# Kernel optimization log

Measured on AMD Instinct MI355X. Metric: run time of the kernel, lower is better.

The kernel has to match this reference:

```python
import jax, jax.numpy as jnp
import numpy as np

NUM_EMBEDDINGS = 1024
EMBEDDING_DIM = 64
COMMITMENT_WEIGHT = 0.25
BATCH = 262144


def setup_inputs() -> dict:
    key = jax.random.key(0)
    k1, k2 = jax.random.split(key)
    z = jax.random.normal(k1, (BATCH, EMBEDDING_DIM), dtype=jnp.float32)
    # torch init: uniform_(-1/K, 1/K)
    bound = 1.0 / NUM_EMBEDDINGS
    codebook = jax.random.uniform(k2, (NUM_EMBEDDINGS, EMBEDDING_DIM), dtype=jnp.float32,
                                  minval=-bound, maxval=bound)
    return {"z": z, "codebook": codebook}


def reference(z, codebook):
    # distances[b, k] = ||z_b||^2 - 2 z_b . c_k + ||c_k||^2   -> [B, K]
    z2 = jnp.sum(z * z, axis=1, keepdims=True)                 # [B, 1]
    c2 = jnp.sum(codebook * codebook, axis=1)                  # [K]
    cross = jnp.matmul(z, codebook.T)                          # [B, K]
    distances = z2 - 2.0 * cross + c2
    indices = jnp.argmin(distances, axis=1)                    # [B]
    # original uses one-hot @ codebook; direct gather is the same math
    z_q = codebook[indices]                                    # [B, D]
    commitment_loss = jnp.mean((jax.lax.stop_gradient(z_q) - z) ** 2)
    codebook_loss = jnp.mean((z_q - jax.lax.stop_gradient(z)) ** 2)
    vq_loss = codebook_loss + COMMITMENT_WEIGHT * commitment_loss
    # straight-through estimator
    z_q_st = z + jax.lax.stop_gradient(z_q - z)
    return z_q_st, vq_loss, indices
```

## Files before the change

kernel.cpp:

```cpp
#include <hip/hip_runtime.h>

#define BATCH   262144
#define NCODE   1024
#define DIM     64
#define BLOCK   256
#define NBLK    (BATCH / BLOCK)
#define MARGIN2 2e-5f
#define QCAP    65536


typedef __attribute__((ext_vector_type(8))) short bf16x8;
typedef __attribute__((ext_vector_type(4))) float f32x4;

#define MFMA(a, b, c) __builtin_amdgcn_mfma_f32_16x16x32_bf16(a, b, c, 0, 0, 0)

__device__ __forceinline__ void split1(float f, unsigned short& h, unsigned short& l) {
    unsigned u = __float_as_uint(f);
    unsigned r = (u + 0x7fffu + ((u >> 16) & 1u)) >> 16;
    h = (unsigned short)r;
    float hf = __uint_as_float(r << 16);
    float lo = f - hf;
    unsigned u2 = __float_as_uint(lo);
    l = (unsigned short)((u2 + 0x7fffu + ((u2 >> 16) & 1u)) >> 16);
}

__global__ __launch_bounds__(256) void prep_kernel(
        const float* __restrict__ cb, float* __restrict__ c2, float* __restrict__ c2n,
        float* __restrict__ cbT, unsigned short* __restrict__ pack,
        unsigned int* __restrict__ qcount, double* __restrict__ dsum,
        unsigned int* __restrict__ dcount)
{
    const int gid = blockIdx.x * 256 + threadIdx.x;
    if (gid == 0) { *qcount = 0u; *dsum = 0.0; *dcount = 0u; }
    cbT[(size_t)(gid & 63) * NCODE + (gid >> 6)] = cb[gid];
    if (gid < NCODE) {
        const float* row = cb + (size_t)gid * DIM;
        float r[8];
#pragma unroll
        for (int j = 0; j < 8; ++j) r[j] = __fmul_rn(row[j], row[j]);
#pragma unroll
        for (int i = 8; i < DIM; i += 8) {
#pragma unroll
            for (int j = 0; j < 8; ++j) r[j] = __fadd_rn(r[j], __fmul_rn(row[i + j], row[i + j]));
        }
        const float v = __fadd_rn(__fadd_rn(__fadd_rn(r[0], r[1]), __fadd_rn(r[2], r[3])),
                                  __fadd_rn(__fadd_rn(r[4], r[5]), __fadd_rn(r[6], r[7])));
        c2[gid] = v;
        c2n[gid] = -0.5f * v;
    }
    if (gid < 4096) {
        const int t = gid >> 6, lane = gid & 63;
        const int c = t * 16 + (lane & 15);
        const int g = lane >> 4;
#pragma unroll
        for (int s = 0; s < 2; ++s) {
            const float* src = cb + (size_t)c * DIM + s * 32 + g * 8;
            bf16x8 hv, lv;
#pragma unroll
            for (int j = 0; j < 8; ++j) {
                unsigned short hh, ll; split1(src[j], hh, ll);
                hv[j] = (short)hh; lv[j] = (short)ll;
            }
            *(bf16x8*)(pack + ((size_t)(t * 4 + 2 * s + 0) * 64 + lane) * 8) = hv;
            *(bf16x8*)(pack + ((size_t)(t * 4 + 2 * s + 1) * 64 + lane) * 8) = lv;
        }
    }
}

__global__ __launch_bounds__(256, 4) void screen_kernel(
        const float* __restrict__ z, const unsigned short* __restrict__ pack,
        const float* __restrict__ c2n, float* __restrict__ out_idx,
        int* __restrict__ queue, unsigned int* __restrict__ qcount)
{
    const int tid  = threadIdx.x;
    const int lane = tid & 63, wid = tid >> 6;
    const int col  = lane & 15, g = lane >> 4;
    const int rowbase = blockIdx.x * 128 + wid * 32;

    bf16x8 Ah[2][2], Al[2][2];
#pragma unroll
    for (int rt = 0; rt < 2; ++rt)
#pragma unroll
        for (int s = 0; s < 2; ++s) {
            const float* zp = z + (size_t)(rowbase + rt * 16 + col) * DIM + s * 32 + g * 8;
            float tmp[8];
            *(float4*)(tmp)     = ((const float4*)zp)[0];
            *(float4*)(tmp + 4) = ((const float4*)zp)[1];
            bf16x8 hv, lv;
#pragma unroll
            for (int j = 0; j < 8; ++j) {
                unsigned short hh, ll; split1(tmp[j], hh, ll);
                hv[j] = (short)hh; lv[j] = (short)ll;
            }
            Ah[rt][s] = hv; Al[rt][s] = lv;
        }

    float b1[8], b2[8], bk[8];
#pragma unroll
    for (int i = 0; i < 8; ++i) {
        b1[i] = -__builtin_inff(); b2[i] = -__builtin_inff(); bk[i] = 0.f;
    }
    float codef = (float)col;

#define UPD(i, sv) { const float s_ = (sv); \
                     bk[i] = (s_ > b1[i]) ? codef : bk[i]; \
                     b2[i] = __builtin_amdgcn_fmed3f(s_, b1[i], b2[i]); \
                     b1[i] = fmaxf(b1[i], s_); }

#define LOADB(BUF, t) { const unsigned short* p_ = pack + (size_t)(t) * 2048 + lane * 8; \
        BUF[0] = *(const bf16x8*)(p_);        BUF[1] = *(const bf16x8*)(p_ +  512); \
        BUF[2] = *(const bf16x8*)(p_ + 1024); BUF[3] = *(const bf16x8*)(p_ + 1536); }

#define COMPUTE(BUF, cv) { \
_Pragma("unroll") \
    for (int rt = 0; rt < 2; ++rt) { \
        f32x4 acc = {cv, cv, cv, cv}; \
        acc = MFMA(Ah[rt][0], BUF[0], acc); acc = MFMA(Ah[rt][1], BUF[2], acc); \
        acc = MFMA(Ah[rt][0], BUF[1], acc); acc = MFMA(Al[rt][0], BUF[0], acc); \
        acc = MFMA(Ah[rt][1], BUF[3], acc); acc = MFMA(Al[rt][1], BUF[2], acc); \
_Pragma("unroll") \
        for (int reg = 0; reg < 4; ++reg) UPD(rt * 4 + reg, acc[reg]); \
    } \
    codef += 16.f; }

    bf16x8 BA[4], BB[4];
    float cA, cB;
    LOADB(BA, 0); cA = c2n[col];
#pragma unroll 1
    for (int tp = 0; tp < 32; ++tp) {
        const int t1 = 2 * tp + 1;
        const int t2 = (t1 < 63) ? t1 + 1 : 63;
        LOADB(BB, t1); cB = c2n[t1 * 16 + col];
        COMPUTE(BA, cA);
        LOADB(BA, t2); cA = c2n[t2 * 16 + col];
        COMPUTE(BB, cB);
    }
#undef COMPUTE
#undef LOADB
#undef UPD

#pragma unroll
    for (int i = 0; i < 8; ++i) {
        float v1 = b1[i], v2 = b2[i], vk = bk[i];
#pragma unroll
        for (int m = 1; m < 16; m <<= 1) {
            const float o1 = __shfl_xor(v1, m);
            const float o2 = __shfl_xor(v2, m);
            const float ok = __shfl_xor(vk, m);
            v2 = fmaxf(fmaxf(v2, o2), fminf(v1, o1));
            if (o1 > v1) vk = ok;
            v1 = fmaxf(v1, o1);
        }
        if (col == 0) {
            const int rt = i >> 2, reg = i & 3;
            const int row = rowbase + rt * 16 + g * 4 + reg;
            out_idx[row] = vk;
            if (v1 - v2 <= MARGIN2) {
                unsigned int p = atomicAdd(qcount, 1u);
                if (p < QCAP) queue[p] = row;
            }
        }
    }
}

__device__ void fix_row(int row, const float* __restrict__ z, const float* __restrict__ cbT,
                        const float* __restrict__ c2, float* __restrict__ out_idx,
                        float* zs, float* rv, int* ri)
{
    const int tid = threadIdx.x;
    __syncthreads();
    if (tid < 16) ((float4*)zs)[tid] = ((const float4*)(z + (size_t)row * DIM))[tid];
    __syncthreads();
    float ra[8];
#pragma unroll
    for (int j = 0; j < 8; ++j) ra[j] = __fmul_rn(zs[j], zs[j]);
#pragma unroll
    for (int d = 8; d < DIM; d += 8) {
#pragma unroll
        for (int j = 0; j < 8; ++j) ra[j] = __fadd_rn(ra[j], __fmul_rn(zs[d + j], zs[d + j]));
    }
    const float z2 = __fadd_rn(__fadd_rn(__fadd_rn(ra[0], ra[1]), __fadd_rn(ra[2], ra[3])),
                               __fadd_rn(__fadd_rn(ra[4], ra[5]), __fadd_rn(ra[6], ra[7])));
    float a[4] = {0.f, 0.f, 0.f, 0.f};
#pragma unroll 8
    for (int d = 0; d < DIM; ++d) {
        const float zd = zs[d];
        const float4 cv = ((const float4*)(cbT + (size_t)d * NCODE))[tid];
        a[0] = __fmaf_rn(zd, cv.x, a[0]);
        a[1] = __fmaf_rn(zd, cv.y, a[1]);
        a[2] = __fmaf_rn(zd, cv.z, a[2]);
        a[3] = __fmaf_rn(zd, cv.w, a[3]);
    }
    const int k0 = tid * 4;
    float best = __builtin_inff();
    int bestk = NCODE;
#pragma unroll
    for (int j = 0; j < 4; ++j) {
        const float dist = __fadd_rn(__fmaf_rn(-2.0f, a[j], z2), c2[k0 + j]);
        if (dist < best) { best = dist; bestk = k0 + j; }
    }
    rv[tid] = best; ri[tid] = bestk;
    __syncthreads();
#pragma unroll
    for (int s = 128; s > 0; s >>= 1) {
        if (tid < s) {
            const float ov = rv[tid + s]; const int oi = ri[tid + s];
            if (ov < rv[tid] || (ov == rv[tid] && oi < ri[tid])) { rv[tid] = ov; ri[tid] = oi; }
        }
        __syncthreads();
    }
    if (tid == 0) out_idx[row] = (float)ri[0];
}

__global__ __launch_bounds__(256) void fix_kernel(
        const float* __restrict__ z, const float* __restrict__ cbT,
        const float* __restrict__ c2, const int* __restrict__ queue,
        const unsigned int* __restrict__ qcount, float* __restrict__ out_idx)
{
    __shared__ float zs[DIM];
    __shared__ float rv[256];
    __shared__ int   ri[256];
    const unsigned int nq = *qcount;
    if (nq <= QCAP) {
        for (unsigned int qi = blockIdx.x; qi < nq; qi += gridDim.x)
            fix_row(queue[qi], z, cbT, c2, out_idx, zs, rv, ri);
    } else {
        for (int row = blockIdx.x; row < BATCH; row += (int)gridDim.x)
            fix_row(row, z, cbT, c2, out_idx, zs, rv, ri);
    }
}

__global__ __launch_bounds__(BLOCK) void emit_kernel(
        const float* __restrict__ z, const float* __restrict__ cb,
        const float* __restrict__ out_idx, float* __restrict__ out_zq,
        double* __restrict__ dsum, unsigned int* __restrict__ dcount,
        float* __restrict__ out_loss)
{
    const int b = blockIdx.x * BLOCK + threadIdx.x;
    const int bestk = (int)out_idx[b];
    const float* cq = cb + (size_t)bestk * DIM;
    const float4* zv = (const float4*)(z + (size_t)b * DIM);
    const float4* qv = (const float4*)cq;
    float4* ov = (float4*)(out_zq + (size_t)b * DIM);
    double lsum = 0.0;
#pragma unroll
    for (int i = 0; i < DIM / 4; ++i) {
        float4 qq = qv[i], zl = zv[i];
        float qa[4] = {qq.x, qq.y, qq.z, qq.w};
        float za[4] = {zl.x, zl.y, zl.z, zl.w};
        float o[4];
#pragma unroll
        for (int j = 0; j < 4; ++j) {
            const float t = __fsub_rn(qa[j], za[j]);
            o[j] = __fadd_rn(za[j], t);
            lsum += (double)t * (double)t;
        }
        float4 vv; vv.x = o[0]; vv.y = o[1]; vv.z = o[2]; vv.w = o[3];
        ov[i] = vv;
    }

    __shared__ double sred[BLOCK];
    sred[threadIdx.x] = lsum;
    __syncthreads();
#pragma unroll
    for (int s = BLOCK / 2; s > 0; s >>= 1) {
        if (threadIdx.x < s) sred[threadIdx.x] += sred[threadIdx.x + s];
        __syncthreads();
    }
    if (threadIdx.x == 0) {
        atomicAdd(dsum, sred[0]);
        __threadfence();
        const unsigned int p = atomicAdd(dcount, 1u);
        if (p == NBLK - 1) {
            __threadfence();
            const double tot = atomicAdd(dsum, 0.0);
            const double mean = tot / (double)((size_t)BATCH * DIM);
            const float L = (float)mean;
            out_loss[0] = __fadd_rn(L, __fmul_rn(0.25f, L));
        }
    }
}

extern "C" void kernel_launch(void* const* d_in, const int* in_sizes, int n_in,
                              void* d_out, int out_size, void* d_ws, size_t ws_size,
                              hipStream_t stream) {
    (void)in_sizes; (void)n_in; (void)out_size; (void)ws_size;
    const float* z  = (const float*)d_in[0];
    const float* cb = (const float*)d_in[1];
    float* out      = (float*)d_out;
    float* out_zq   = out;
    float* out_loss = out + (size_t)BATCH * DIM;
    float* out_idx  = out + (size_t)BATCH * DIM + 1;
    double* dsum    = (double*)d_ws;
    unsigned int* dcount = (unsigned int*)((char*)d_ws + 8);
    unsigned int* qcount = (unsigned int*)((char*)d_ws + 12);
    float* c2       = (float*)((char*)d_ws + 1024);
    float* c2n      = (float*)((char*)d_ws + 5120);
    unsigned short* pack = (unsigned short*)((char*)d_ws + 16384);
    int* queue      = (int*)((char*)d_ws + 278528);
    float* cbT      = (float*)((char*)d_ws + 540672);

    prep_kernel<<<256, 256, 0, stream>>>(cb, c2, c2n, cbT, pack, qcount, dsum, dcount);
    screen_kernel<<<BATCH / 128, 256, 0, stream>>>(z, pack, c2n, out_idx, queue, qcount);
    fix_kernel<<<2048, 256, 0, stream>>>(z, cbT, c2, queue, qcount, out_idx);
    emit_kernel<<<NBLK, BLOCK, 0, stream>>>(z, cb, out_idx, out_zq, dsum, dcount, out_loss);
}
```

Before: 368.2 us.

## Double rows per wave and stage codebook tiles through LDS asynchronously

```diff
diff --git a/kernel.cpp b/kernel.cpp
--- a/kernel.cpp
+++ b/kernel.cpp
@@ -67,19 +67,23 @@
     }
 }
 
-__global__ __launch_bounds__(256, 4) void screen_kernel(
+__global__ __launch_bounds__(256, 3) void screen_kernel(
         const float* __restrict__ z, const unsigned short* __restrict__ pack,
         const float* __restrict__ c2n, float* __restrict__ out_idx,
         int* __restrict__ queue, unsigned int* __restrict__ qcount)
 {
+    __shared__ __align__(16) unsigned short ldsb[4][2][2048];
+    __shared__ float c2s[NCODE];
     const int tid  = threadIdx.x;
     const int lane = tid & 63, wid = tid >> 6;
     const int col  = lane & 15, g = lane >> 4;
-    const int rowbase = blockIdx.x * 128 + wid * 32;
-
-    bf16x8 Ah[2][2], Al[2][2];
-#pragma unroll
-    for (int rt = 0; rt < 2; ++rt)
+    const int rowbase = blockIdx.x * 256 + wid * 64;
+
+    ((float4*)c2s)[tid] = ((const float4*)c2n)[tid];
+
+    bf16x8 Ah[4][2], Al[4][2];
+#pragma unroll
+    for (int rt = 0; rt < 4; ++rt)
 #pragma unroll
         for (int s = 0; s < 2; ++s) {
             const float* zp = z + (size_t)(rowbase + rt * 16 + col) * DIM + s * 32 + g * 8;
@@ -95,9 +99,9 @@
             Ah[rt][s] = hv; Al[rt][s] = lv;
         }
 
-    float b1[8], b2[8], bk[8];
-#pragma unroll
-    for (int i = 0; i < 8; ++i) {
+    float b1[16], b2[16], bk[16];
+#pragma unroll
+    for (int i = 0; i < 16; ++i) {
         b1[i] = -__builtin_inff(); b2[i] = -__builtin_inff(); bk[i] = 0.f;
     }
     float codef = (float)col;
@@ -107,40 +111,45 @@
                      b2[i] = __builtin_amdgcn_fmed3f(s_, b1[i], b2[i]); \
                      b1[i] = fmaxf(b1[i], s_); }
 
-#define LOADB(BUF, t) { const unsigned short* p_ = pack + (size_t)(t) * 2048 + lane * 8; \
-        BUF[0] = *(const bf16x8*)(p_);        BUF[1] = *(const bf16x8*)(p_ +  512); \
-        BUF[2] = *(const bf16x8*)(p_ + 1024); BUF[3] = *(const bf16x8*)(p_ + 1536); }
-
-#define COMPUTE(BUF, cv) { \
+#define STAGE(t, buf) { \
 _Pragma("unroll") \
-    for (int rt = 0; rt < 2; ++rt) { \
-        f32x4 acc = {cv, cv, cv, cv}; \
-        acc = MFMA(Ah[rt][0], BUF[0], acc); acc = MFMA(Ah[rt][1], BUF[2], acc); \
-        acc = MFMA(Ah[rt][0], BUF[1], acc); acc = MFMA(Al[rt][0], BUF[0], acc); \
-        acc = MFMA(Ah[rt][1], BUF[3], acc); acc = MFMA(Al[rt][1], BUF[2], acc); \
-_Pragma("unroll") \
-        for (int reg = 0; reg < 4; ++reg) UPD(rt * 4 + reg, acc[reg]); \
-    } \
-    codef += 16.f; }
-
-    bf16x8 BA[4], BB[4];
-    float cA, cB;
-    LOADB(BA, 0); cA = c2n[col];
+        for (int i_ = 0; i_ < 4; ++i_) { \
+            const unsigned short* g_ = pack + (size_t)(t) * 2048 + i_ * 512 + lane * 8; \
+            unsigned short* l_ = &ldsb[wid][buf][i_ * 512]; \
+            __builtin_amdgcn_global_load_lds( \
+                (const __attribute__((address_space(1))) unsigned int*)g_, \
+                (__attribute__((address_space(3))) unsigned int*)l_, 16, 0, 0); \
+        } }
+
+    STAGE(0, 0);
+    __syncthreads();
 #pragma unroll 1
-    for (int tp = 0; tp < 32; ++tp) {
-        const int t1 = 2 * tp + 1;
-        const int t2 = (t1 < 63) ? t1 + 1 : 63;
-        LOADB(BB, t1); cB = c2n[t1 * 16 + col];
-        COMPUTE(BA, cA);
-        LOADB(BA, t2); cA = c2n[t2 * 16 + col];
-        COMPUTE(BB, cB);
-    }
-#undef COMPUTE
-#undef LOADB
+    for (int t = 0; t < 64; ++t) {
+        const int cur = t & 1;
+        asm volatile("s_waitcnt vmcnt(0)" ::: "memory");
+        const unsigned short* lb = &ldsb[wid][cur][0];
+        bf16x8 B0 = *(const bf16x8*)(lb +    0 + lane * 8);
+        bf16x8 B1 = *(const bf16x8*)(lb +  512 + lane * 8);
+        bf16x8 B2 = *(const bf16x8*)(lb + 1024 + lane * 8);
+        bf16x8 B3 = *(const bf16x8*)(lb + 1536 + lane * 8);
+        if (t < 63) STAGE(t + 1, cur ^ 1);
+        const float cv = c2s[t * 16 + col];
+#pragma unroll
+        for (int rt = 0; rt < 4; ++rt) {
+            f32x4 acc = {cv, cv, cv, cv};
+            acc = MFMA(Ah[rt][0], B0, acc); acc = MFMA(Ah[rt][1], B2, acc);
+            acc = MFMA(Ah[rt][0], B1, acc); acc = MFMA(Al[rt][0], B0, acc);
+            acc = MFMA(Ah[rt][1], B3, acc); acc = MFMA(Al[rt][1], B2, acc);
+#pragma unroll
+            for (int reg = 0; reg < 4; ++reg) UPD(rt * 4 + reg, acc[reg]);
+        }
+        codef += 16.f;
+    }
 #undef UPD
-
-#pragma unroll
-    for (int i = 0; i < 8; ++i) {
+#undef STAGE
+
+#pragma unroll
+    for (int i = 0; i < 16; ++i) {
         float v1 = b1[i], v2 = b2[i], vk = bk[i];
 #pragma unroll
         for (int m = 1; m < 16; m <<= 1) {
@@ -301,7 +310,7 @@
     float* cbT      = (float*)((char*)d_ws + 540672);
 
     prep_kernel<<<256, 256, 0, stream>>>(cb, c2, c2n, cbT, pack, qcount, dsum, dcount);
-    screen_kernel<<<BATCH / 128, 256, 0, stream>>>(z, pack, c2n, out_idx, queue, qcount);
+    screen_kernel<<<BATCH / 256, 256, 0, stream>>>(z, pack, c2n, out_idx, queue, qcount);
     fix_kernel<<<2048, 256, 0, stream>>>(z, cbT, c2, queue, qcount, out_idx);
     emit_kernel<<<NBLK, BLOCK, 0, stream>>>(z, cb, out_idx, out_zq, dsum, dcount, out_loss);
 }
```

Result: no change. 363.3 us (-1.3%).
